# Performance work log

Measured on AMD Instinct MI355X. Metric: run time of the kernel, lower is better.

Reference implementation:

```python
import jax, jax.numpy as jnp
import numpy as np

B, C_IN, C_OUT, N_LOW, N_UP, K = 16, 256, 128, 10242, 40962, 7  # ico order 5 -> 6, 1-ring size 7


def setup_inputs() -> dict:
    key = jax.random.key(0)
    k1, k2, k3 = jax.random.split(key, 3)
    x = jax.random.normal(k1, (B, C_IN, N_LOW), dtype=jnp.float32)
    # nn.Linear(in_feats, K*out_feats); stored as [in, K*out] for einsum
    weight = jax.random.normal(k2, (C_IN, K * C_OUT), dtype=jnp.float32) * 0.05
    bias = jax.random.normal(k3, (K * C_OUT,), dtype=jnp.float32) * 0.05
    # flat neighbor indices must cover every up-level vertex at least once
    rng = np.random.default_rng(0)
    cover = rng.permutation(N_UP)
    extra = rng.integers(0, N_UP, size=N_LOW * K - N_UP)
    neigh_flat = jnp.asarray(np.concatenate([cover, extra]).astype(np.int32))
    return {"x": x, "weight": weight, "bias": bias,
            "neigh_flat": neigh_flat, "n_up": N_UP}


def reference(x, weight, bias, neigh_flat, n_up):
    # x: [B, C_in, V] -> per-vertex linear expand to [B, V, K*C_out]
    Bn, _, V = x.shape
    y = jnp.einsum('bcv,cf->bvf', x, weight) + bias
    y = y.reshape(Bn, V * K, C_OUT)            # [B, V*K, C_out]
    y = jnp.transpose(y, (1, 0, 2))            # [V*K, B, C_out] segment axis first
    sums = jax.ops.segment_sum(y, neigh_flat, num_segments=n_up)      # [n_up, B, C_out]
    counts = jax.ops.segment_sum(jnp.ones((V * K,), y.dtype), neigh_flat,
                                 num_segments=n_up)                    # [n_up]
    out = sums / counts[:, None, None]         # mean over variable-size groups
    return jnp.transpose(out, (1, 2, 0))       # [B, C_out, n_up]
```

## Files before the change

### kernel.cpp

```cpp
#include <hip/hip_runtime.h>
#include <stdint.h>

#define B_    16
#define CIN   256
#define COUT  128
#define VLOW  10242
#define NUP   40962
#define KTAP  7
#define FTOT  (KTAP * COUT)
#define VK    (VLOW * KTAP)
#define NBLK  41
#define VPAD  10368

typedef __attribute__((ext_vector_type(4))) float  floatx4;
typedef __attribute__((ext_vector_type(8))) short  bf16x8;

typedef __attribute__((address_space(3))) unsigned char       lds_u8;
typedef const __attribute__((address_space(1))) unsigned char gbl_u8;

__device__ __forceinline__ void gl_lds16(const unsigned short* g, unsigned short* l) {
    __builtin_amdgcn_global_load_lds((gbl_u8*)g, (lds_u8*)l, 16, 0, 0);
}

__device__ __forceinline__ unsigned short f2bf(float f) {
    union { float f; unsigned int u; } x; x.f = f;
    unsigned int r = x.u + 0x7FFFu + ((x.u >> 16) & 1u);
    return (unsigned short)(r >> 16);
}
__device__ __forceinline__ float bflo(unsigned int u) {
    union { unsigned int u; float f; } x; x.u = u << 16; return x.f;
}
__device__ __forceinline__ float bfhi(unsigned int u) {
    union { unsigned int u; float f; } x; x.u = u & 0xFFFF0000u; return x.f;
}


__global__ void count_kernel(const int* __restrict__ neigh, int* __restrict__ counts) {
    int i = blockIdx.x * blockDim.x + threadIdx.x;
    if (i < VK) atomicAdd(&counts[neigh[i]], 1);
}

__global__ __launch_bounds__(1024)
void scan_local(const int* __restrict__ counts, int* __restrict__ offs, int* __restrict__ bsum) {
    __shared__ int s[1024];
    const int t = threadIdx.x;
    const int idx = blockIdx.x * 1024 + t;
    int v = (idx < NUP) ? counts[idx] : 0;
    s[t] = v;
    __syncthreads();
    int acc = v;
    for (int off = 1; off < 1024; off <<= 1) {
        int add = (t >= off) ? s[t - off] : 0;
        __syncthreads();
        acc += add;
        s[t] = acc;
        __syncthreads();
    }
    if (idx < NUP) offs[idx] = acc - v;
    if (t == 1023) bsum[blockIdx.x] = acc;
}

__global__ void scan_sums(const int* __restrict__ bsum, int* __restrict__ bbase) {
    if (threadIdx.x == 0) {
        int r = 0;
        for (int j = 0; j < NBLK; ++j) { bbase[j] = r; r += bsum[j]; }
    }
}

__global__ void fill_csr(const int* __restrict__ neigh, const int* __restrict__ offs,
                         const int* __restrict__ bbase, int* __restrict__ cursor,
                         int* __restrict__ csr) {
    int i = blockIdx.x * blockDim.x + threadIdx.x;
    if (i < VK) {
        int n = neigh[i];
        int p = atomicAdd(&cursor[n], 1);
        csr[offs[n] + bbase[n >> 10] + p] = i;
    }
}

__global__ __launch_bounds__(256)
void transpose256(const float* __restrict__ src, unsigned short* __restrict__ dst,
                  int C, int CLIM, int CPAD)
{
    __shared__ unsigned short lt[64][72];
    const int t  = threadIdx.x;
    const int v0 = blockIdx.x * 64;
    const int c0 = blockIdx.y * 64;
    const int z  = blockIdx.z;
    const float* s = src + (size_t)z * 256 * C;
    unsigned short* d = dst + (size_t)z * CPAD * 256;

#pragma unroll
    for (int p = 0; p < 16; ++p) {
        int cr = c0 + p * 4 + (t >> 6);
        int v  = v0 + (t & 63);
        float val = (v < CLIM) ? s[(size_t)cr * C + v] : 0.0f;
        lt[t & 63][p * 4 + (t >> 6)] = f2bf(val);
    }
    __syncthreads();
#pragma unroll
    for (int p = 0; p < 2; ++p) {
        int vl = p * 32 + (t >> 3);
        int v  = v0 + vl;
        if (v < CPAD) {
            uint4 val = *(const uint4*)&lt[vl][(t & 7) * 8];
            *(uint4*)&d[(size_t)v * 256 + c0 + (t & 7) * 8] = val;
        }
    }
}

__global__ __launch_bounds__(256)
void gemm_y(const unsigned short* __restrict__ xT,
            const unsigned short* __restrict__ wT,
            const float* __restrict__ bias,
            unsigned short* __restrict__ y)
{
    __shared__ unsigned short smem[8320];
    unsigned short* lds_a = smem;
    unsigned short* lds_b = smem + 4096;

    const int t    = threadIdx.x;
    const int vt   = blockIdx.x;
    const int ktap = blockIdx.y;
    const int bl   = blockIdx.z;
    const int v0   = vt * 128;
    const int f0   = ktap * 128;

    const int lane = t & 63;
    const int wid  = t >> 6;
    const int wv   = wid & 1;
    const int wf   = wid >> 1;
    const int mrow = lane & 15;
    const int quad = lane >> 4;
    const int kb   = quad * 8;

    floatx4 acc[4][4];
#pragma unroll
    for (int i = 0; i < 4; i++)
#pragma unroll
        for (int j = 0; j < 4; j++) acc[i][j] = (floatx4)0.0f;

    const int srow = (lane >> 2);
    const int scol = (lane & 3) << 3;
    const unsigned short* gA0 = xT + (((size_t)bl * VPAD + v0 + (2 * wid) * 16 + srow) << 8) + scol;
    const unsigned short* gA1 = gA0 + (16 << 8);
    const unsigned short* gB0 = wT + (((size_t)f0 + (2 * wid) * 16 + srow) << 8) + scol;
    const unsigned short* gB1 = gB0 + (16 << 8);
    unsigned short* lA0 = lds_a + (2 * wid) * 512;
    unsigned short* lA1 = lA0 + 512;
    unsigned short* lB0 = lds_b + (2 * wid) * 512;
    unsigned short* lB1 = lB0 + 512;

    for (int kc = 0; kc < CIN; kc += 32) {
        __syncthreads();
        gl_lds16(gA0 + kc, lA0);
        gl_lds16(gA1 + kc, lA1);
        gl_lds16(gB0 + kc, lB0);
        gl_lds16(gB1 + kc, lB1);
        __syncthreads();

        bf16x8 fa[4], fb[4];
#pragma unroll
        for (int i = 0; i < 4; i++)
            fa[i] = *(const bf16x8*)&lds_a[(wv * 64 + i * 16 + mrow) * 32 + kb];
#pragma unroll
        for (int j = 0; j < 4; j++)
            fb[j] = *(const bf16x8*)&lds_b[(wf * 64 + j * 16 + mrow) * 32 + kb];
#pragma unroll
        for (int i = 0; i < 4; i++)
#pragma unroll
            for (int j = 0; j < 4; j++)
                acc[i][j] = __builtin_amdgcn_mfma_f32_16x16x32_bf16(fa[i], fb[j], acc[i][j], 0, 0, 0);
    }

    float bvv[4];
#pragma unroll
    for (int j = 0; j < 4; j++) bvv[j] = bias[f0 + wf * 64 + j * 16 + mrow];

    unsigned short* yb = y + (size_t)bl * VLOW * FTOT;
#pragma unroll
    for (int half = 0; half < 2; ++half) {
        __syncthreads();
        if (wv == half) {
#pragma unroll
            for (int i = 0; i < 4; i++)
#pragma unroll
                for (int j = 0; j < 4; j++)
#pragma unroll
                    for (int r = 0; r < 4; r++) {
                        int vl = i * 16 + quad * 4 + r;
                        int c  = wf * 64 + j * 16 + mrow;
                        smem[vl * 130 + c] = f2bf(acc[i][j][r] + bvv[j]);
                    }
        }
        __syncthreads();
        int row = t >> 2, cb = (t & 3) * 32;
        int v = v0 + half * 64 + row;
        if (v < VLOW) {
            unsigned int tmp[16];
#pragma unroll
            for (int q = 0; q < 16; q++)
                tmp[q] = *(const unsigned int*)&smem[row * 130 + cb + q * 2];
            uint4* dst = (uint4*)(yb + (size_t)v * FTOT + f0 + cb);
            dst[0] = make_uint4(tmp[0],  tmp[1],  tmp[2],  tmp[3]);
            dst[1] = make_uint4(tmp[4],  tmp[5],  tmp[6],  tmp[7]);
            dst[2] = make_uint4(tmp[8],  tmp[9],  tmp[10], tmp[11]);
            dst[3] = make_uint4(tmp[12], tmp[13], tmp[14], tmp[15]);
        }
    }
}

__global__ __launch_bounds__(256)
void gather_out(const unsigned short* __restrict__ y, const int* __restrict__ offs,
                const int* __restrict__ bbase, const int* __restrict__ counts,
                const int* __restrict__ csr, float* __restrict__ out, int b_base)
{
    __shared__ float lt[64 * 130];
    const int t = threadIdx.x, lane = t & 63, wvv = t >> 6;
    const int n0 = blockIdx.x * 64;
    const int bl = blockIdx.y;
    const unsigned short* yb = y + (size_t)bl * VLOW * FTOT;

    for (int nl = 0; nl < 16; ++nl) {
        int nloc = wvv * 16 + nl;
        int n = n0 + nloc;
        float a0 = 0.0f, a1 = 0.0f;
        if (n < NUP) {
            int st  = offs[n] + bbase[n >> 10];
            int cnt = counts[n];
            for (int e = 0; e < cnt; ++e) {
                int i = csr[st + e];
                int v = i / 7, k = i - v * 7;
                unsigned int u = *(const unsigned int*)(yb + (size_t)v * FTOT + k * COUT + lane * 2);
                a0 += bflo(u);
                a1 += bfhi(u);
            }
            float inv = cnt ? 1.0f / (float)cnt : 0.0f;
            a0 *= inv; a1 *= inv;
        }
        lt[nloc * 130 + lane * 2]     = a0;
        lt[nloc * 130 + lane * 2 + 1] = a1;
    }
    __syncthreads();

    float* ob = out + (size_t)(b_base + bl) * COUT * NUP;
    int nl2 = t & 63, n = n0 + nl2;
    if (n < NUP) {
#pragma unroll
        for (int rr = 0; rr < 32; ++rr) {
            int c = rr * 4 + (t >> 6);
            ob[(size_t)c * NUP + n] = lt[nl2 * 130 + c];
        }
    }
}


extern "C" void kernel_launch(void* const* d_in, const int* in_sizes, int n_in,
                              void* d_out, int out_size, void* d_ws, size_t ws_size,
                              hipStream_t stream) {
    const float* x     = (const float*)d_in[0];
    const float* w     = (const float*)d_in[1];
    const float* bias  = (const float*)d_in[2];
    const int*   neigh = (const int*)d_in[3];
    float* out = (float*)d_out;

    char* p = (char*)d_ws;
    const size_t a_nup = ((size_t)NUP * 4 + 255) & ~(size_t)255;
    int* counts = (int*)p;           p += a_nup;
    int* cursor = (int*)p;           p += a_nup;
    int* offs   = (int*)p;           p += a_nup;
    int* bsum   = (int*)p;           p += 256;
    int* bbase  = (int*)p;           p += 256;
    int* csr    = (int*)p;           p += ((size_t)VK * 4 + 255) & ~(size_t)255;
    unsigned short* wT = (unsigned short*)p;  p += ((size_t)FTOT * 256 * 2 + 255) & ~(size_t)255;

    size_t meta    = (size_t)(p - (char*)d_ws);
    size_t xT_per  = (size_t)VPAD * 256 * 2;
    size_t y_per   = (size_t)VLOW * FTOT * 2;
    int G = 4;
    while (G > 1 && meta + (size_t)G * (xT_per + y_per) > ws_size) G >>= 1;

    unsigned short* xT = (unsigned short*)p;
    unsigned short* y  = (unsigned short*)(p + (size_t)G * xT_per);

    hipMemsetAsync(counts, 0, a_nup * 2, stream);

    count_kernel<<<(VK + 255) / 256, 256, 0, stream>>>(neigh, counts);
    scan_local<<<NBLK, 1024, 0, stream>>>(counts, offs, bsum);
    scan_sums<<<1, 64, 0, stream>>>(bsum, bbase);
    fill_csr<<<(VK + 255) / 256, 256, 0, stream>>>(neigh, offs, bbase, cursor, csr);
    transpose256<<<dim3(FTOT / 64, 4, 1), 256, 0, stream>>>(w, wT, FTOT, FTOT, FTOT);

    for (int bg = 0; bg < B_; bg += G) {
        transpose256<<<dim3(VPAD / 64, 4, G), 256, 0, stream>>>(
            x + (size_t)bg * CIN * VLOW, xT, VLOW, VLOW, VPAD);
        gemm_y<<<dim3(81, KTAP, G), 256, 0, stream>>>(xT, wT, bias, y);
        gather_out<<<dim3(641, G), 256, 0, stream>>>(y, offs, bbase, counts, csr, out, bg);
    }
}
```

Before: 1.012 ms.

## Double-buffer GEMM LDS staging, stage CSR in LDS for gather, enlarge batch group

The GEMM now uses two LDS buffers so global-to-LDS loads for the next K chunk are issued while the current chunk feeds the MFMAs, which removes one barrier per iteration. The gather kernel reads a precomputed CSR position array, stages the block's CSR segment in shared memory, indexes y directly as i*128 without a divide by 7, and unrolls the edge loop by two. The batch group size can grow to 16 when the workspace allows, which cuts the number of kernel launches. The costs are double the GEMM shared memory, which may lower occupancy, and a larger workspace footprint.

```diff
diff --git a/kernel.cpp b/kernel.cpp
--- a/kernel.cpp
+++ b/kernel.cpp
@@ -11,6 +11,7 @@
 #define VK    (VLOW * KTAP)
 #define NBLK  41
 #define VPAD  10368
+#define CSR_CAP 512
 
 typedef __attribute__((ext_vector_type(4))) float  floatx4;
 typedef __attribute__((ext_vector_type(8))) short  bf16x8;
@@ -61,9 +62,13 @@
 }
 
 __global__ void scan_sums(const int* __restrict__ bsum, int* __restrict__ bbase) {
-    if (threadIdx.x == 0) {
+    __shared__ int s[64];
+    int t = threadIdx.x;
+    s[t] = (t < NBLK) ? bsum[t] : 0;
+    __syncthreads();
+    if (t == 0) {
         int r = 0;
-        for (int j = 0; j < NBLK; ++j) { bbase[j] = r; r += bsum[j]; }
+        for (int j = 0; j < NBLK; ++j) { bbase[j] = r; r += s[j]; }
     }
 }
 
@@ -76,6 +81,12 @@
         int p = atomicAdd(&cursor[n], 1);
         csr[offs[n] + bbase[n >> 10] + p] = i;
     }
+}
+
+__global__ void make_pos(const int* __restrict__ offs, const int* __restrict__ bbase,
+                         int* __restrict__ pos) {
+    int i = blockIdx.x * blockDim.x + threadIdx.x;
+    if (i <= NUP) pos[i] = (i < NUP) ? (offs[i] + bbase[i >> 10]) : VK;
 }
 
 __global__ __launch_bounds__(256)
@@ -115,9 +126,11 @@
             const float* __restrict__ bias,
             unsigned short* __restrict__ y)
 {
-    __shared__ unsigned short smem[8320];
-    unsigned short* lds_a = smem;
-    unsigned short* lds_b = smem + 4096;
+    __shared__ unsigned short smem[16384];
+    unsigned short* A0 = smem;
+    unsigned short* B0 = smem + 4096;
+    unsigned short* A1 = smem + 8192;
+    unsigned short* B1 = smem + 12288;
 
     const int t    = threadIdx.x;
     const int vt   = blockIdx.x;
@@ -142,36 +155,49 @@
 
     const int srow = (lane >> 2);
     const int scol = (lane & 3) << 3;
-    const unsigned short* gA0 = xT + (((size_t)bl * VPAD + v0 + (2 * wid) * 16 + srow) << 8) + scol;
+    const unsigned short* gA0 = xT + (((size_t)bl * VPAD + v0 + wid * 32 + srow) << 8) + scol;
     const unsigned short* gA1 = gA0 + (16 << 8);
-    const unsigned short* gB0 = wT + (((size_t)f0 + (2 * wid) * 16 + srow) << 8) + scol;
+    const unsigned short* gB0 = wT + (((size_t)f0 + wid * 32 + srow) << 8) + scol;
     const unsigned short* gB1 = gB0 + (16 << 8);
-    unsigned short* lA0 = lds_a + (2 * wid) * 512;
-    unsigned short* lA1 = lA0 + 512;
-    unsigned short* lB0 = lds_b + (2 * wid) * 512;
-    unsigned short* lB1 = lB0 + 512;
-
-    for (int kc = 0; kc < CIN; kc += 32) {
-        __syncthreads();
-        gl_lds16(gA0 + kc, lA0);
-        gl_lds16(gA1 + kc, lA1);
-        gl_lds16(gB0 + kc, lB0);
-        gl_lds16(gB1 + kc, lB1);
-        __syncthreads();
-
-        bf16x8 fa[4], fb[4];
-#pragma unroll
-        for (int i = 0; i < 4; i++)
-            fa[i] = *(const bf16x8*)&lds_a[(wv * 64 + i * 16 + mrow) * 32 + kb];
-#pragma unroll
-        for (int j = 0; j < 4; j++)
-            fb[j] = *(const bf16x8*)&lds_b[(wf * 64 + j * 16 + mrow) * 32 + kb];
-#pragma unroll
-        for (int i = 0; i < 4; i++)
-#pragma unroll
-            for (int j = 0; j < 4; j++)
-                acc[i][j] = __builtin_amdgcn_mfma_f32_16x16x32_bf16(fa[i], fb[j], acc[i][j], 0, 0, 0);
-    }
+    const int woff = wid * 1024;
+
+#define STAGE(AB, BB, KC) do {                        \
+        gl_lds16(gA0 + (KC), (AB) + woff);            \
+        gl_lds16(gA1 + (KC), (AB) + woff + 512);      \
+        gl_lds16(gB0 + (KC), (BB) + woff);            \
+        gl_lds16(gB1 + (KC), (BB) + woff + 512);      \
+    } while (0)
+
+#define COMPUTE(AB, BB) do {                                                        \
+        bf16x8 fa[4], fb[4];                                                        \
+        _Pragma("unroll")                                                           \
+        for (int i = 0; i < 4; i++)                                                 \
+            fa[i] = *(const bf16x8*)&(AB)[(wv * 64 + i * 16 + mrow) * 32 + kb];     \
+        _Pragma("unroll")                                                           \
+        for (int j = 0; j < 4; j++)                                                 \
+            fb[j] = *(const bf16x8*)&(BB)[(wf * 64 + j * 16 + mrow) * 32 + kb];     \
+        _Pragma("unroll")                                                           \
+        for (int i = 0; i < 4; i++)                                                 \
+            _Pragma("unroll")                                                       \
+            for (int j = 0; j < 4; j++)                                             \
+                acc[i][j] = __builtin_amdgcn_mfma_f32_16x16x32_bf16(fa[i], fb[j],   \
+                                                                    acc[i][j], 0, 0, 0); \
+    } while (0)
+
+    STAGE(A0, B0, 0);
+    __syncthreads();
+#pragma unroll
+    for (int tt = 0; tt < 4; ++tt) {
+        const int kc = tt * 64;
+        if (kc + 32 < CIN) STAGE(A1, B1, kc + 32);
+        COMPUTE(A0, B0);
+        __syncthreads();
+        if (kc + 64 < CIN) STAGE(A0, B0, kc + 64);
+        COMPUTE(A1, B1);
+        __syncthreads();
+    }
+#undef STAGE
+#undef COMPUTE
 
     float bvv[4];
 #pragma unroll
@@ -211,39 +237,56 @@
 }
 
 __global__ __launch_bounds__(256)
-void gather_out(const unsigned short* __restrict__ y, const int* __restrict__ offs,
-                const int* __restrict__ bbase, const int* __restrict__ counts,
-                const int* __restrict__ csr, float* __restrict__ out, int b_base)
+void gather_out(const unsigned short* __restrict__ y, const int* __restrict__ pos,
+                const int* __restrict__ csr, float* __restrict__ out)
 {
+    __shared__ int   s_pos[65];
+    __shared__ int   s_csr[CSR_CAP];
     __shared__ float lt[64 * 130];
     const int t = threadIdx.x, lane = t & 63, wvv = t >> 6;
     const int n0 = blockIdx.x * 64;
     const int bl = blockIdx.y;
     const unsigned short* yb = y + (size_t)bl * VLOW * FTOT;
 
+    if (t < 65) {
+        int idx = n0 + t; if (idx > NUP) idx = NUP;
+        s_pos[t] = pos[idx];
+    }
+    __syncthreads();
+    const int S = s_pos[0];
+    const int num = s_pos[64] - S;
+    const bool fits = (num <= CSR_CAP);
+    if (fits) for (int i = t; i < num; i += 256) s_csr[i] = csr[S + i];
+    __syncthreads();
+
+#pragma unroll
     for (int nl = 0; nl < 16; ++nl) {
-        int nloc = wvv * 16 + nl;
-        int n = n0 + nloc;
+        const int nloc = wvv * 16 + nl;
+        const int st  = s_pos[nloc] - S;
+        const int cnt = s_pos[nloc + 1] - s_pos[nloc];
         float a0 = 0.0f, a1 = 0.0f;
-        if (n < NUP) {
-            int st  = offs[n] + bbase[n >> 10];
-            int cnt = counts[n];
-            for (int e = 0; e < cnt; ++e) {
-                int i = csr[st + e];
-                int v = i / 7, k = i - v * 7;
-                unsigned int u = *(const unsigned int*)(yb + (size_t)v * FTOT + k * COUT + lane * 2);
-                a0 += bflo(u);
-                a1 += bfhi(u);
-            }
-            float inv = cnt ? 1.0f / (float)cnt : 0.0f;
-            a0 *= inv; a1 *= inv;
-        }
-        lt[nloc * 130 + lane * 2]     = a0;
-        lt[nloc * 130 + lane * 2 + 1] = a1;
-    }
-    __syncthreads();
-
-    float* ob = out + (size_t)(b_base + bl) * COUT * NUP;
+        int e = 0;
+        for (; e + 2 <= cnt; e += 2) {
+            int i0 = fits ? s_csr[st + e]     : csr[S + st + e];
+            int i1 = fits ? s_csr[st + e + 1] : csr[S + st + e + 1];
+            unsigned u0 = *(const unsigned int*)(yb + (((size_t)i0) << 7) + lane * 2);
+            unsigned u1 = *(const unsigned int*)(yb + (((size_t)i1) << 7) + lane * 2);
+            a0 += bflo(u0) + bflo(u1);
+            a1 += bfhi(u0) + bfhi(u1);
+        }
+        if (e < cnt) {
+            int i0 = fits ? s_csr[st + e] : csr[S + st + e];
+            unsigned u0 = *(const unsigned int*)(yb + (((size_t)i0) << 7) + lane * 2);
+            a0 += bflo(u0);
+            a1 += bfhi(u0);
+        }
+        float inv = cnt ? 1.0f / (float)cnt : 0.0f;
+        lt[nloc * 130 + lane * 2]     = a0 * inv;
+        lt[nloc * 130 + lane * 2 + 1] = a1 * inv;
+    }
+    __syncthreads();
+
+    float* ob = out + (size_t)bl * COUT * NUP;
     int nl2 = t & 63, n = n0 + nl2;
     if (n < NUP) {
 #pragma unroll
@@ -269,6 +312,7 @@
     int* counts = (int*)p;           p += a_nup;
     int* cursor = (int*)p;           p += a_nup;
     int* offs   = (int*)p;           p += a_nup;
+    int* pos    = (int*)p;           p += a_nup + 256;
     int* bsum   = (int*)p;           p += 256;
     int* bbase  = (int*)p;           p += 256;
     int* csr    = (int*)p;           p += ((size_t)VK * 4 + 255) & ~(size_t)255;
@@ -277,7 +321,7 @@
     size_t meta    = (size_t)(p - (char*)d_ws);
     size_t xT_per  = (size_t)VPAD * 256 * 2;
     size_t y_per   = (size_t)VLOW * FTOT * 2;
-    int G = 4;
+    int G = 16;
     while (G > 1 && meta + (size_t)G * (xT_per + y_per) > ws_size) G >>= 1;
 
     unsigned short* xT = (unsigned short*)p;
@@ -289,12 +333,14 @@
     scan_local<<<NBLK, 1024, 0, stream>>>(counts, offs, bsum);
     scan_sums<<<1, 64, 0, stream>>>(bsum, bbase);
     fill_csr<<<(VK + 255) / 256, 256, 0, stream>>>(neigh, offs, bbase, cursor, csr);
+    make_pos<<<(NUP + 256) / 256, 256, 0, stream>>>(offs, bbase, pos);
     transpose256<<<dim3(FTOT / 64, 4, 1), 256, 0, stream>>>(w, wT, FTOT, FTOT, FTOT);
 
     for (int bg = 0; bg < B_; bg += G) {
         transpose256<<<dim3(VPAD / 64, 4, G), 256, 0, stream>>>(
             x + (size_t)bg * CIN * VLOW, xT, VLOW, VLOW, VPAD);
         gemm_y<<<dim3(81, KTAP, G), 256, 0, stream>>>(xT, wT, bias, y);
-        gather_out<<<dim3(641, G), 256, 0, stream>>>(y, offs, bbase, counts, csr, out, bg);
-    }
-}
+        gather_out<<<dim3(641, G), 256, 0, stream>>>(
+            y, pos, csr, out + (size_t)bg * COUT * NUP);
+    }
+}
```

New measurement: 881.2 us. 1.15x faster.
